# Optimization experiments

Measured on AMD Instinct MI355X. Metric: run time of the kernel, lower is better.

Reference implementation:

```python
import jax, jax.numpy as jnp
import numpy as np

HEAD = 16
DIM = 1024
HEAD_DIM = DIM // HEAD


def setup_inputs() -> dict:
    key = jax.random.key(0)
    k1, k2, k3, k4 = jax.random.split(key, 4)
    x = jax.random.normal(k1, (2, 2048, DIM), dtype=jnp.float32)
    # nn.Linear(dim, 3*dim, bias=False): weight [3*dim, dim]
    w_qkv = jax.random.normal(k2, (3 * DIM, DIM), dtype=jnp.float32) * (DIM ** -0.5)
    # output proj nn.Linear(dim, dim)
    w_out = jax.random.normal(k3, (DIM, DIM), dtype=jnp.float32) * (DIM ** -0.5)
    b_out = jax.random.normal(k4, (DIM,), dtype=jnp.float32) * 0.01
    return {"x": x, "w_qkv": w_qkv, "w_out": w_out, "b_out": b_out}


def reference(x, w_qkv, w_out, b_out):
    b, s, _ = x.shape
    scale = HEAD_DIM ** -0.5
    qkv = jnp.einsum('bsd,ed->bse', x, w_qkv)  # [b, s, 3*dim]
    q, k, v = jnp.split(qkv, 3, axis=-1)
    def split_heads(t):
        return t.reshape(b, s, HEAD, HEAD_DIM).transpose(0, 2, 1, 3)  # b h s d
    q, k, v = split_heads(q), split_heads(k), split_heads(v)
    scores = jnp.einsum('bhqd,bhkd->bhqk', q, k) * scale
    attn = jax.nn.softmax(scores, axis=-1)
    out = jnp.einsum('bhqk,bhkd->bhqd', attn, v)
    out = out.transpose(0, 2, 1, 3).reshape(b, s, DIM)
    out = jnp.einsum('bsd,ed->bse', out, w_out) + b_out
    return out
```

## Files before the change

kernel.cpp:

```cpp
#include <hip/hip_runtime.h>
#include <hip/hip_bf16.h>
#include <stdint.h>

typedef __bf16 bf16_t;
typedef __attribute__((ext_vector_type(8))) __bf16 bf16x8;
typedef __attribute__((ext_vector_type(4))) __bf16 bf16x4v;
typedef __attribute__((ext_vector_type(4))) float f32x4;

#define GLOBAL_AS __attribute__((address_space(1)))
#define LDS_AS __attribute__((address_space(3)))

__device__ __forceinline__ void gload_lds16(const bf16_t* g, bf16_t* l) {
  __builtin_amdgcn_global_load_lds((const GLOBAL_AS void*)g, (LDS_AS void*)l, 16, 0, 0);
}

__device__ __forceinline__ uint32_t pk2(float a, float b) {
  union { bf16_t h[2]; uint32_t u; } x;
  x.h[0] = (bf16_t)a; x.h[1] = (bf16_t)b;
  return x.u;
}

__device__ __forceinline__ bf16x8 xpose8(bf16x8 v, int l) {
  union { bf16x8 v; uint32_t u[4]; } tv; tv.v = v;
  uint32_t a0 = __shfl_xor((int)tv.u[2], 4, 64);
  uint32_t a1 = __shfl_xor((int)tv.u[3], 4, 64);
  uint32_t a2 = __shfl_xor((int)tv.u[0], 4, 64);
  uint32_t a3 = __shfl_xor((int)tv.u[1], 4, 64);
  bool s4 = (l & 4) != 0;
  uint32_t n0 = s4 ? a0 : tv.u[0];
  uint32_t n1 = s4 ? a1 : tv.u[1];
  uint32_t n2 = s4 ? tv.u[2] : a2;
  uint32_t n3 = s4 ? tv.u[3] : a3;
  uint32_t b0 = __shfl_xor((int)n1, 2, 64);
  uint32_t b1 = __shfl_xor((int)n0, 2, 64);
  uint32_t b2 = __shfl_xor((int)n3, 2, 64);
  uint32_t b3 = __shfl_xor((int)n2, 2, 64);
  bool s2 = (l & 2) != 0;
  uint32_t m0 = s2 ? b0 : n0;
  uint32_t m1 = s2 ? n1 : b1;
  uint32_t m2 = s2 ? b2 : n2;
  uint32_t m3 = s2 ? n3 : b3;
  uint32_t c0 = __shfl_xor((int)m0, 1, 64);
  uint32_t c1 = __shfl_xor((int)m1, 1, 64);
  uint32_t c2 = __shfl_xor((int)m2, 1, 64);
  uint32_t c3 = __shfl_xor((int)m3, 1, 64);
  bool odd = (l & 1) != 0;
  union { uint32_t u[4]; bf16x8 v; } tw;
  tw.u[0] = odd ? ((m0 & 0xFFFF0000u) | (c0 >> 16)) : ((m0 & 0xFFFFu) | (c0 << 16));
  tw.u[1] = odd ? ((m1 & 0xFFFF0000u) | (c1 >> 16)) : ((m1 & 0xFFFFu) | (c1 << 16));
  tw.u[2] = odd ? ((m2 & 0xFFFF0000u) | (c2 >> 16)) : ((m2 & 0xFFFFu) | (c2 << 16));
  tw.u[3] = odd ? ((m3 & 0xFFFF0000u) | (c3 >> 16)) : ((m3 & 0xFFFFu) | (c3 << 16));
  return tw.v;
}

__global__ void cvt_f32_bf16(const float* __restrict__ in, bf16_t* __restrict__ out, int n) {
  int i = (blockIdx.x * 256 + threadIdx.x) * 4;
  if (i + 3 < n) {
    float4 v = *(const float4*)(in + i);
    bf16x4v o;
    o[0] = (bf16_t)v.x; o[1] = (bf16_t)v.y; o[2] = (bf16_t)v.z; o[3] = (bf16_t)v.w;
    *(bf16x4v*)(out + i) = o;
  }
}

template<int EPI>
__global__ __launch_bounds__(256)
void gemm_tn(const bf16_t* __restrict__ A, const bf16_t* __restrict__ B,
             void* __restrict__ Cout, const float* __restrict__ bias,
             int K, int ldc, int qcols, float qscale)
{
  __shared__ __align__(16) bf16_t As[128 * 32];
  __shared__ __align__(16) bf16_t Bs[128 * 32];
  const int t  = threadIdx.x;
  const int l  = t & 63, w = t >> 6;
  const int wm = w >> 1, wn = w & 1;
  const int lo = l & 15, hi = l >> 4;
  const int brow = blockIdx.y * 128;
  const int bcol = blockIdx.x * 128;

  const int i0 = t, i1 = t + 256;
  const int r0 = i0 >> 2, c0 = i0 & 3;
  const int r1 = i1 >> 2, c1 = i1 & 3;

  f32x4 acc[4][4] = {};

  for (int k0 = 0; k0 < K; k0 += 32) {
    gload_lds16(A + (size_t)(brow + r0) * K + k0 + c0 * 8, As + i0 * 8);
    gload_lds16(A + (size_t)(brow + r1) * K + k0 + c1 * 8, As + i1 * 8);
    gload_lds16(B + (size_t)(bcol + r0) * K + k0 + c0 * 8, Bs + i0 * 8);
    gload_lds16(B + (size_t)(bcol + r1) * K + k0 + c1 * 8, Bs + i1 * 8);
    __syncthreads();

    bf16x8 a[4], bb[4];
#pragma unroll
    for (int fm = 0; fm < 4; fm++)
      a[fm] = *(const bf16x8*)(As + (wm * 64 + fm * 16 + lo) * 32 + hi * 8);
#pragma unroll
    for (int fn = 0; fn < 4; fn++)
      bb[fn] = *(const bf16x8*)(Bs + (wn * 64 + fn * 16 + lo) * 32 + hi * 8);

#pragma unroll
    for (int fm = 0; fm < 4; fm++)
#pragma unroll
      for (int fn = 0; fn < 4; fn++)
        acc[fm][fn] = __builtin_amdgcn_mfma_f32_16x16x32_bf16(a[fm], bb[fn], acc[fm][fn], 0, 0, 0);
    __syncthreads();
  }

#pragma unroll
  for (int fm = 0; fm < 4; fm++) {
#pragma unroll
    for (int fn = 0; fn < 4; fn++) {
#pragma unroll
      for (int j = 0; j < 4; j++) {
        int row = brow + wm * 64 + fm * 16 + hi * 4 + j;
        int col = bcol + wn * 64 + fn * 16 + lo;
        float v = acc[fm][fn][j];
        if (EPI == 0) {
          if (col < qcols) v *= qscale;
          ((bf16_t*)Cout)[(size_t)row * ldc + col] = (bf16_t)v;
        } else {
          ((float*)Cout)[(size_t)row * ldc + col] = v + bias[col];
        }
      }
    }
  }
}

#define LDK  72
#define LDKV 136

__global__ __launch_bounds__(512, 2)
void flash_attn(const bf16_t* __restrict__ qkv, bf16_t* __restrict__ aout)
{
  __shared__ __align__(16) bf16_t Kl[2][128 * LDK];
  __shared__ __align__(16) bf16_t Vt[2][64 * LDKV];

  const int t = threadIdx.x;
  const int l = t & 63, w = t >> 6;
  const int lo = l & 15, hi = l >> 4;
  int bid = (int)blockIdx.x;
  bid = (bid & 7) * 64 + (bid >> 3);
  const int qblk = bid & 15;
  const int bh   = bid >> 4;
  const int b = bh >> 4, h = bh & 15;
  const int rowbase = b * 2048;
  const int q0 = qblk * 128 + w * 16;

  const int r = l & 7, c = l >> 3;
  const int krow = w * 8 + (l >> 3);
  const int kc   = l & 7;
  const int vkey = 32 * (w >> 2) + 16 * (r >> 2) + 4 * (w & 3) + (r & 3);
  const bf16_t* kvbase = qkv + (size_t)rowbase * 3072 + h * 64 + 1024;
  const size_t step = (size_t)128 * 3072;

  bf16x8 aq[2];
#pragma unroll
  for (int kb = 0; kb < 2; kb++)
    aq[kb] = *(const bf16x8*)(qkv + (size_t)(rowbase + q0 + lo) * 3072
                              + h * 64 + kb * 32 + hi * 8);

  bf16x8 ones;
#pragma unroll
  for (int j = 0; j < 8; j++) ones[j] = (bf16_t)1.0f;

  f32x4 oacc[4] = {};
  f32x4 ssum = {};

  bf16x8 kch[2], vch[2];
#pragma unroll
  for (int i = 0; i < 2; i++) {
    kch[i] = *(const bf16x8*)(kvbase + (size_t)(krow + 64 * i) * 3072 + kc * 8);
    vch[i] = *(const bf16x8*)(kvbase + 1024 + (size_t)(vkey + 64 * i) * 3072 + c * 8);
  }
#pragma unroll
  for (int i = 0; i < 2; i++) {
    *(bf16x8*)(&Kl[0][0] + (krow + 64 * i) * LDK + kc * 8) = kch[i];
    *(bf16x8*)(&Vt[0][0] + (c * 8 + r) * LDKV + 64 * i + w * 8) = xpose8(vch[i], l);
  }
  const bf16_t* kv_next = kvbase + step;
#pragma unroll
  for (int i = 0; i < 2; i++) {
    kch[i] = *(const bf16x8*)(kv_next + (size_t)(krow + 64 * i) * 3072 + kc * 8);
    vch[i] = *(const bf16x8*)(kv_next + 1024 + (size_t)(vkey + 64 * i) * 3072 + c * 8);
  }
  kv_next += step;

  for (int it = 0; it < 16; ++it) {
    __syncthreads();
    const int cur = it & 1;
    bf16_t* KlN = &Kl[cur ^ 1][0];
    bf16_t* VtN = &Vt[cur ^ 1][0];
    const bf16_t* KlC = &Kl[cur][0];
    const bf16_t* VtC = &Vt[cur][0];

    if (it < 15) {
#pragma unroll
      for (int i = 0; i < 2; i++) {
        *(bf16x8*)(KlN + (krow + 64 * i) * LDK + kc * 8) = kch[i];
        *(bf16x8*)(VtN + (c * 8 + r) * LDKV + 64 * i + w * 8) = xpose8(vch[i], l);
      }
    }
    if (it < 14) {
#pragma unroll
      for (int i = 0; i < 2; i++) {
        kch[i] = *(const bf16x8*)(kv_next + (size_t)(krow + 64 * i) * 3072 + kc * 8);
        vch[i] = *(const bf16x8*)(kv_next + 1024 + (size_t)(vkey + 64 * i) * 3072 + c * 8);
      }
      kv_next += step;
    }

#pragma unroll
    for (int h2 = 0; h2 < 2; h2++) {
      bf16x8 kf[4][2];
#pragma unroll
      for (int fn = 0; fn < 4; fn++)
#pragma unroll
        for (int kb = 0; kb < 2; kb++)
          kf[fn][kb] = *(const bf16x8*)(KlC + (64 * h2 + fn * 16 + lo) * LDK + kb * 32 + hi * 8);
      f32x4 sacc[4] = {};
      __builtin_amdgcn_s_setprio(1);
#pragma unroll
      for (int fn = 0; fn < 4; fn++)
#pragma unroll
        for (int kb = 0; kb < 2; kb++)
          sacc[fn] = __builtin_amdgcn_mfma_f32_16x16x32_bf16(kf[fn][kb], aq[kb], sacc[fn], 0, 0, 0);
      __builtin_amdgcn_s_setprio(0);

      float p[4][4];
#pragma unroll
      for (int fn = 0; fn < 4; fn++)
#pragma unroll
        for (int j = 0; j < 4; j++)
          p[fn][j] = __builtin_amdgcn_exp2f(sacc[fn][j]);
      bf16x8 pa[2];
#pragma unroll
      for (int kb = 0; kb < 2; kb++) {
        union { uint32_t u[4]; bf16x8 v; } pw;
        pw.u[0] = pk2(p[2 * kb][0],     p[2 * kb][1]);
        pw.u[1] = pk2(p[2 * kb][2],     p[2 * kb][3]);
        pw.u[2] = pk2(p[2 * kb + 1][0], p[2 * kb + 1][1]);
        pw.u[3] = pk2(p[2 * kb + 1][2], p[2 * kb + 1][3]);
        pa[kb] = pw.v;
      }

      bf16x8 vb[4][2];
#pragma unroll
      for (int fd = 0; fd < 4; fd++)
#pragma unroll
        for (int kb = 0; kb < 2; kb++)
          vb[fd][kb] = *(const bf16x8*)(VtC + (fd * 16 + lo) * LDKV + 64 * h2 + kb * 32 + hi * 8);
      __builtin_amdgcn_s_setprio(1);
#pragma unroll
      for (int kb = 0; kb < 2; kb++)
        ssum = __builtin_amdgcn_mfma_f32_16x16x32_bf16(pa[kb], ones, ssum, 0, 0, 0);
#pragma unroll
      for (int fd = 0; fd < 4; fd++)
#pragma unroll
        for (int kb = 0; kb < 2; kb++)
          oacc[fd] = __builtin_amdgcn_mfma_f32_16x16x32_bf16(pa[kb], vb[fd][kb], oacc[fd], 0, 0, 0);
      __builtin_amdgcn_s_setprio(0);
    }
  }

#pragma unroll
  for (int j = 0; j < 4; j++) {
    float inv = 1.0f / ssum[j];
    int row = rowbase + q0 + hi * 4 + j;
#pragma unroll
    for (int fd = 0; fd < 4; fd++) {
      int col = h * 64 + fd * 16 + lo;
      aout[(size_t)row * 1024 + col] = (bf16_t)(oacc[fd][j] * inv);
    }
  }
}

extern "C" void kernel_launch(void* const* d_in, const int* in_sizes, int n_in,
                              void* d_out, int out_size, void* d_ws, size_t ws_size,
                              hipStream_t stream) {
  const float* x     = (const float*)d_in[0];
  const float* w_qkv = (const float*)d_in[1];
  const float* w_out = (const float*)d_in[2];
  const float* b_out = (const float*)d_in[3];

  char* ws = (char*)d_ws;
  bf16_t* xb   = (bf16_t*)(ws);
  bf16_t* wqb  = (bf16_t*)(ws + 8388608);
  bf16_t* wob  = (bf16_t*)(ws + 14680064);
  bf16_t* qkvb = (bf16_t*)(ws + 16777216);
  bf16_t* aob  = (bf16_t*)(ws + 41943040);

  cvt_f32_bf16<<<4096, 256, 0, stream>>>(x,     xb,  4194304);
  cvt_f32_bf16<<<3072, 256, 0, stream>>>(w_qkv, wqb, 3145728);
  cvt_f32_bf16<<<1024, 256, 0, stream>>>(w_out, wob, 1048576);

  dim3 g1(24, 32);
  gemm_tn<0><<<g1, 256, 0, stream>>>(xb, wqb, qkvb, nullptr, 1024, 3072, 1024, 0.18033688011f);

  flash_attn<<<512, 512, 0, stream>>>(qkvb, aob);

  dim3 g2(8, 32);
  gemm_tn<1><<<g2, 256, 0, stream>>>(aob, wob, d_out, b_out, 1024, 1024, 0, 1.0f);
}
```

Baseline: 140.8 us.

## Merge conversion launches, swizzle GEMM blocks per XCD, drop MFMA setprio

The three fp32-to-bf16 conversion kernels become one launch that picks its source buffer by index range. This relies on xb, wqb and wob being laid out contiguously in the workspace. The GEMMs switch to a 1D grid whose block ids are remapped so that consecutive ids on each of the 8 XCDs cover neighbouring tiles, aiming for better L2 reuse. The s_setprio hints around the attention MFMAs are also removed, which changes how waves are scheduled against each other.

Result: faster. 135.2 us (-4.0%).

```diff
diff --git a/kernel.cpp b/kernel.cpp
--- a/kernel.cpp
+++ b/kernel.cpp
@@ -53,21 +53,25 @@
   return tw.v;
 }
 
-__global__ void cvt_f32_bf16(const float* __restrict__ in, bf16_t* __restrict__ out, int n) {
+__global__ void cvt3_f32_bf16(const float* __restrict__ x, const float* __restrict__ wq,
+                              const float* __restrict__ wo, bf16_t* __restrict__ out) {
   int i = (blockIdx.x * 256 + threadIdx.x) * 4;
-  if (i + 3 < n) {
-    float4 v = *(const float4*)(in + i);
-    bf16x4v o;
-    o[0] = (bf16_t)v.x; o[1] = (bf16_t)v.y; o[2] = (bf16_t)v.z; o[3] = (bf16_t)v.w;
-    *(bf16x4v*)(out + i) = o;
-  }
+  const float* src;
+  int off;
+  if (i < 4194304)      { src = x;  off = 0; }
+  else if (i < 7340032) { src = wq; off = 4194304; }
+  else                  { src = wo; off = 7340032; }
+  float4 v = *(const float4*)(src + (i - off));
+  bf16x4v o;
+  o[0] = (bf16_t)v.x; o[1] = (bf16_t)v.y; o[2] = (bf16_t)v.z; o[3] = (bf16_t)v.w;
+  *(bf16x4v*)(out + i) = o;
 }
 
 template<int EPI>
 __global__ __launch_bounds__(256)
 void gemm_tn(const bf16_t* __restrict__ A, const bf16_t* __restrict__ B,
              void* __restrict__ Cout, const float* __restrict__ bias,
-             int K, int ldc, int qcols, float qscale)
+             int K, int ldc, int qcols, float qscale, int nbx, int cpx)
 {
   __shared__ __align__(16) bf16_t As[128 * 32];
   __shared__ __align__(16) bf16_t Bs[128 * 32];
@@ -75,8 +79,10 @@
   const int l  = t & 63, w = t >> 6;
   const int wm = w >> 1, wn = w & 1;
   const int lo = l & 15, hi = l >> 4;
-  const int brow = blockIdx.y * 128;
-  const int bcol = blockIdx.x * 128;
+  int bid = (int)blockIdx.x;
+  bid = (bid & 7) * cpx + (bid >> 3);
+  const int brow = (bid / nbx) * 128;
+  const int bcol = (bid % nbx) * 128;
 
   const int i0 = t, i1 = t + 256;
   const int r0 = i0 >> 2, c0 = i0 & 3;
@@ -219,13 +225,11 @@
         for (int kb = 0; kb < 2; kb++)
           kf[fn][kb] = *(const bf16x8*)(KlC + (64 * h2 + fn * 16 + lo) * LDK + kb * 32 + hi * 8);
       f32x4 sacc[4] = {};
-      __builtin_amdgcn_s_setprio(1);
 #pragma unroll
       for (int fn = 0; fn < 4; fn++)
 #pragma unroll
         for (int kb = 0; kb < 2; kb++)
           sacc[fn] = __builtin_amdgcn_mfma_f32_16x16x32_bf16(kf[fn][kb], aq[kb], sacc[fn], 0, 0, 0);
-      __builtin_amdgcn_s_setprio(0);
 
       float p[4][4];
 #pragma unroll
@@ -250,7 +254,6 @@
 #pragma unroll
         for (int kb = 0; kb < 2; kb++)
           vb[fd][kb] = *(const bf16x8*)(VtC + (fd * 16 + lo) * LDKV + 64 * h2 + kb * 32 + hi * 8);
-      __builtin_amdgcn_s_setprio(1);
 #pragma unroll
       for (int kb = 0; kb < 2; kb++)
         ssum = __builtin_amdgcn_mfma_f32_16x16x32_bf16(pa[kb], ones, ssum, 0, 0, 0);
@@ -259,7 +262,6 @@
 #pragma unroll
         for (int kb = 0; kb < 2; kb++)
           oacc[fd] = __builtin_amdgcn_mfma_f32_16x16x32_bf16(pa[kb], vb[fd][kb], oacc[fd], 0, 0, 0);
-      __builtin_amdgcn_s_setprio(0);
     }
   }
 
@@ -290,15 +292,13 @@
   bf16_t* qkvb = (bf16_t*)(ws + 16777216);
   bf16_t* aob  = (bf16_t*)(ws + 41943040);
 
-  cvt_f32_bf16<<<4096, 256, 0, stream>>>(x,     xb,  4194304);
-  cvt_f32_bf16<<<3072, 256, 0, stream>>>(w_qkv, wqb, 3145728);
-  cvt_f32_bf16<<<1024, 256, 0, stream>>>(w_out, wob, 1048576);
-
-  dim3 g1(24, 32);
-  gemm_tn<0><<<g1, 256, 0, stream>>>(xb, wqb, qkvb, nullptr, 1024, 3072, 1024, 0.18033688011f);
+  cvt3_f32_bf16<<<8192, 256, 0, stream>>>(x, w_qkv, w_out, xb);
+
+  gemm_tn<0><<<768, 256, 0, stream>>>(xb, wqb, qkvb, nullptr, 1024, 3072,
+                                      1024, 0.18033688011f, 24, 96);
 
   flash_attn<<<512, 512, 0, stream>>>(qkvb, aob);
 
-  dim3 g2(8, 32);
-  gemm_tn<1><<<g2, 256, 0, stream>>>(aob, wob, d_out, b_out, 1024, 1024, 0, 1.0f);
-}
+  gemm_tn<1><<<256, 256, 0, stream>>>(aob, wob, d_out, b_out, 1024, 1024,
+                                      0, 1.0f, 8, 32);
+}
```
